# Performance work log

Measured on AMD Instinct MI355X. Metric: run time of the kernel, lower is better.

## Reference

```python
import jax, jax.numpy as jnp
import numpy as np

T, H, S = 131072, 768, 16384
MAX_LEN = 32


def setup_inputs() -> dict:
    key = jax.random.key(0)
    k1, k2, k3, k4 = jax.random.split(key, 4)
    token_emb = jax.random.normal(k1, (T, H), dtype=jnp.float32)
    # spans: start in [0, T-MAX_LEN), length in [1, MAX_LEN], end exclusive
    starts = jax.random.randint(k2, (S,), 0, T - MAX_LEN)
    lengths = jax.random.randint(k3, (S,), 1, MAX_LEN + 1)
    spans = jnp.stack([starts, starts + lengths], axis=1).astype(jnp.int64)
    kw1, kw2 = jax.random.split(k4)
    W1 = jax.random.normal(kw1, (3 * H, H), dtype=jnp.float32) * (1.0 / np.sqrt(3 * H))
    b1 = jnp.zeros((H,), dtype=jnp.float32)
    W2 = jax.random.normal(kw2, (H, H), dtype=jnp.float32) * (1.0 / np.sqrt(H))
    b2 = jnp.zeros((H,), dtype=jnp.float32)
    return {"token_emb": token_emb, "spans": spans, "W1": W1, "b1": b1, "W2": W2, "b2": b2}


def reference(token_emb, spans, W1, b1, W2, b2):
    starts = spans[:, 0]          # [S]
    ends = spans[:, 1]           # [S], exclusive
    h_start = token_emb[starts]   # [S, H]
    h_end = token_emb[ends - 1]   # [S, H]
    # ragged mean over h[s:e] via exclusive-prefix-sum difference
    zeros = jnp.zeros((1, token_emb.shape[1]), dtype=token_emb.dtype)
    cs = jnp.concatenate([zeros, jnp.cumsum(token_emb, axis=0)], axis=0)  # [T+1, H]
    lengths = (ends - starts).astype(token_emb.dtype)[:, None]            # [S, 1]
    h_mean = (cs[ends] - cs[starts]) / lengths                            # [S, H]
    feat = jnp.concatenate([h_start, h_end, h_mean], axis=-1)            # [S, 3H]
    # span_proj: Linear(3H->H) + GELU (dropout = identity at eval)
    z = jax.nn.gelu(feat @ W1 + b1, approximate=False)
    # projector: Linear(H->proj_dim) + GELU
    return jax.nn.gelu(z @ W2 + b2, approximate=False)
```

## Files before the change

kernel.cpp:

```cpp
#include <hip/hip_runtime.h>
#include <hip/hip_bf16.h>
#include <math.h>

#define H_DIM   768
#define S_SPAN  16384
#define K1_DIM  2304

typedef __attribute__((ext_vector_type(8))) short short8;
typedef __attribute__((ext_vector_type(4))) float floatx4;

__device__ __forceinline__ float gelu_exact(float x) {
    return 0.5f * x * (1.0f + erff(x * 0.70710678118654752f));
}

__device__ __forceinline__ void async_ld16(const __hip_bfloat16* g, __hip_bfloat16* l) {
    __builtin_amdgcn_global_load_lds(
        (const __attribute__((address_space(1))) void*)g,
        (__attribute__((address_space(3))) void*)l, 16, 0, 0);
}

__device__ __forceinline__ void store_out(float* p, float v) { *p = v; }
__device__ __forceinline__ void store_out(__hip_bfloat16* p, float v) { *p = __float2bfloat16(v); }

__global__ void transpose_to_bf16(const float* __restrict__ src,
                                  __hip_bfloat16* __restrict__ dst,
                                  int K, int N) {
    __shared__ float tile[32][33];
    const int nb = blockIdx.x * 32;
    const int kb = blockIdx.y * 32;
    const int tx = threadIdx.x;
    const int ty = threadIdx.y;
#pragma unroll
    for (int i = ty; i < 32; i += 8)
        tile[i][tx] = src[(size_t)(kb + i) * N + nb + tx];
    __syncthreads();
#pragma unroll
    for (int i = ty; i < 32; i += 8)
        dst[(size_t)(nb + i) * K + kb + tx] = __float2bfloat16(tile[tx][i]);
}

__global__ __launch_bounds__(192)
void gather_feat(const float* __restrict__ emb,
                 const int* __restrict__ spans,
                 __hip_bfloat16* __restrict__ feat) {
    const int s = blockIdx.x;
    const int st = spans[2 * s];
    const int en = spans[2 * s + 1];
    const int len = en - st;
    const int t = threadIdx.x;

    const float4* p = (const float4*)(emb + (size_t)st * H_DIM) + t;
    float4 v = *p;
    float4 first = v;
    float4 last = v;
    float sx = v.x, sy = v.y, sz = v.z, sw = v.w;
    for (int i = 1; i < len; ++i) {
        p += (H_DIM / 4);
        v = *p;
        sx += v.x; sy += v.y; sz += v.z; sw += v.w;
        last = v;
    }
    const float inv = 1.0f / (float)len;

    __hip_bfloat16* f = feat + (size_t)s * K1_DIM + 4 * t;
    union { __hip_bfloat16 h[4]; uint2 u; } pk;
    pk.h[0] = __float2bfloat16(first.x); pk.h[1] = __float2bfloat16(first.y);
    pk.h[2] = __float2bfloat16(first.z); pk.h[3] = __float2bfloat16(first.w);
    *(uint2*)(f) = pk.u;
    pk.h[0] = __float2bfloat16(last.x);  pk.h[1] = __float2bfloat16(last.y);
    pk.h[2] = __float2bfloat16(last.z);  pk.h[3] = __float2bfloat16(last.w);
    *(uint2*)(f + H_DIM) = pk.u;
    pk.h[0] = __float2bfloat16(sx * inv); pk.h[1] = __float2bfloat16(sy * inv);
    pk.h[2] = __float2bfloat16(sz * inv); pk.h[3] = __float2bfloat16(sw * inv);
    *(uint2*)(f + 2 * H_DIM) = pk.u;
}

template <typename OutT>
__global__ __launch_bounds__(256, 3)
void gemm_bias_gelu(const __hip_bfloat16* __restrict__ A,
                    const __hip_bfloat16* __restrict__ Bt,
                    const float* __restrict__ bias,
                    OutT* __restrict__ C,
                    int M, int N, int K) {
    __shared__ __align__(16) __hip_bfloat16 sA[128 * 32];
    __shared__ __align__(16) __hip_bfloat16 sB[128 * 32];

    const int tid  = threadIdx.x;
    const int wave = tid >> 6;
    const int lane = tid & 63;
    const int waveM = (wave >> 1) * 64;
    const int waveN = (wave & 1) * 64;

    const int tm0 = blockIdx.y * 128;
    const int tn0 = blockIdx.x * 128;

    const __hip_bfloat16* Abase = A + (size_t)tm0 * K;
    const __hip_bfloat16* Bbase = Bt + (size_t)tn0 * K;

    const int srow = wave * 32 + (lane >> 2);
    const int skof = (lane & 3) * 8;
    const __hip_bfloat16* gA0 = Abase + (size_t)srow * K + skof;
    const __hip_bfloat16* gA1 = gA0 + (size_t)16 * K;
    const __hip_bfloat16* gB0 = Bbase + (size_t)srow * K + skof;
    const __hip_bfloat16* gB1 = gB0 + (size_t)16 * K;
    __hip_bfloat16* lA0 = &sA[wave * 1024];
    __hip_bfloat16* lA1 = &sA[wave * 1024 + 512];
    __hip_bfloat16* lB0 = &sB[wave * 1024];
    __hip_bfloat16* lB1 = &sB[wave * 1024 + 512];

    floatx4 acc[4][4] = {};

    const int fr = lane & 15;
    const int fq = (lane >> 4) * 8;

    for (int k0 = 0; k0 < K; k0 += 32) {
        __syncthreads();
        async_ld16(gA0 + k0, lA0);
        async_ld16(gA1 + k0, lA1);
        async_ld16(gB0 + k0, lB0);
        async_ld16(gB1 + k0, lB1);
        __syncthreads();

        short8 af[4], bfr[4];
#pragma unroll
        for (int i = 0; i < 4; ++i) {
            af[i]  = *(const short8*)&sA[(waveM + i * 16 + fr) * 32 + fq];
            bfr[i] = *(const short8*)&sB[(waveN + i * 16 + fr) * 32 + fq];
        }
#pragma unroll
        for (int mi = 0; mi < 4; ++mi)
#pragma unroll
            for (int ni = 0; ni < 4; ++ni)
                acc[mi][ni] = __builtin_amdgcn_mfma_f32_16x16x32_bf16(
                    af[mi], bfr[ni], acc[mi][ni], 0, 0, 0);
    }

    const int col = lane & 15;
    const int rq  = (lane >> 4) * 4;
#pragma unroll
    for (int ni = 0; ni < 4; ++ni) {
        const int gc = tn0 + waveN + ni * 16 + col;
        const float bv = bias[gc];
#pragma unroll
        for (int mi = 0; mi < 4; ++mi) {
#pragma unroll
            for (int r = 0; r < 4; ++r) {
                const int gr = tm0 + waveM + mi * 16 + rq + r;
                store_out(&C[(size_t)gr * N + gc], gelu_exact(acc[mi][ni][r] + bv));
            }
        }
    }
}

extern "C" void kernel_launch(void* const* d_in, const int* in_sizes, int n_in,
                              void* d_out, int out_size, void* d_ws, size_t ws_size,
                              hipStream_t stream) {
    const float* token_emb = (const float*)d_in[0];
    const int*   spans     = (const int*)d_in[1];
    const float* W1        = (const float*)d_in[2];
    const float* b1        = (const float*)d_in[3];
    const float* W2        = (const float*)d_in[4];
    const float* b2        = (const float*)d_in[5];
    float*       out       = (float*)d_out;

    __hip_bfloat16* W1t  = (__hip_bfloat16*)d_ws;
    __hip_bfloat16* W2t  = W1t  + (size_t)H_DIM * K1_DIM;
    __hip_bfloat16* feat = W2t  + (size_t)H_DIM * H_DIM;
    __hip_bfloat16* z    = feat + (size_t)S_SPAN * K1_DIM;

    transpose_to_bf16<<<dim3(H_DIM / 32, K1_DIM / 32), dim3(32, 8), 0, stream>>>(
        W1, W1t, K1_DIM, H_DIM);
    transpose_to_bf16<<<dim3(H_DIM / 32, H_DIM / 32), dim3(32, 8), 0, stream>>>(
        W2, W2t, H_DIM, H_DIM);
    gather_feat<<<S_SPAN, 192, 0, stream>>>(token_emb, spans, feat);
    gemm_bias_gelu<__hip_bfloat16><<<dim3(H_DIM / 128, S_SPAN / 128), 256, 0, stream>>>(
        feat, W1t, b1, z, S_SPAN, H_DIM, K1_DIM);
    gemm_bias_gelu<float><<<dim3(H_DIM / 128, S_SPAN / 128), 256, 0, stream>>>(
        z, W2t, b2, out, S_SPAN, H_DIM, H_DIM);
}
```

Measured before the change: 728.1 us.

## Use one wave per span in gather with prefetch, and remap GEMM blocks across XCDs

The gather kernel now gives each span a single 64-lane wave that handles three float4 per lane, and software-prefetches the next row while accumulating the current one. This gives each thread more independent loads in flight and cuts the number of blocks launched. The GEMM swizzles the linear block id so that consecutive blocks on the same XCD cover neighbouring M rows and share all N tiles, which is meant to improve L2 reuse of the A panels. The prefetch always reads one row past the span end; with the input generation used here that row stays inside the table, but it is an extra load.

```diff
diff --git a/kernel.cpp b/kernel.cpp
--- a/kernel.cpp
+++ b/kernel.cpp
@@ -39,40 +39,55 @@
         dst[(size_t)(nb + i) * K + kb + tx] = __float2bfloat16(tile[tx][i]);
 }
 
-__global__ __launch_bounds__(192)
+__device__ __forceinline__ void store_row3(__hip_bfloat16* f, int lane,
+                                           float4 v0, float4 v1, float4 v2) {
+    union { __hip_bfloat16 h[4]; uint2 u; } pk;
+    pk.h[0] = __float2bfloat16(v0.x); pk.h[1] = __float2bfloat16(v0.y);
+    pk.h[2] = __float2bfloat16(v0.z); pk.h[3] = __float2bfloat16(v0.w);
+    *(uint2*)(f + 4 * lane) = pk.u;
+    pk.h[0] = __float2bfloat16(v1.x); pk.h[1] = __float2bfloat16(v1.y);
+    pk.h[2] = __float2bfloat16(v1.z); pk.h[3] = __float2bfloat16(v1.w);
+    *(uint2*)(f + 4 * (lane + 64)) = pk.u;
+    pk.h[0] = __float2bfloat16(v2.x); pk.h[1] = __float2bfloat16(v2.y);
+    pk.h[2] = __float2bfloat16(v2.z); pk.h[3] = __float2bfloat16(v2.w);
+    *(uint2*)(f + 4 * (lane + 128)) = pk.u;
+}
+
+__global__ __launch_bounds__(256)
 void gather_feat(const float* __restrict__ emb,
                  const int* __restrict__ spans,
                  __hip_bfloat16* __restrict__ feat) {
-    const int s = blockIdx.x;
-    const int st = spans[2 * s];
-    const int en = spans[2 * s + 1];
-    const int len = en - st;
-    const int t = threadIdx.x;
+    const int s    = blockIdx.x * 4 + (threadIdx.x >> 6);
+    const int lane = threadIdx.x & 63;
+    const int st   = spans[2 * s];
+    const int len  = spans[2 * s + 1] - st;
 
-    const float4* p = (const float4*)(emb + (size_t)st * H_DIM) + t;
-    float4 v = *p;
-    float4 first = v;
-    float4 last = v;
-    float sx = v.x, sy = v.y, sz = v.z, sw = v.w;
+    const float4* r = (const float4*)(emb + (size_t)st * H_DIM);
+    float4 a0 = r[lane], a1 = r[lane + 64], a2 = r[lane + 128];
+
+    __hip_bfloat16* f = feat + (size_t)s * K1_DIM;
+    store_row3(f, lane, a0, a1, a2);
+
+    float4 s0 = a0, s1 = a1, s2 = a2;
+    r += H_DIM / 4;
+    float4 n0 = r[lane], n1 = r[lane + 64], n2 = r[lane + 128];
+
     for (int i = 1; i < len; ++i) {
-        p += (H_DIM / 4);
-        v = *p;
-        sx += v.x; sy += v.y; sz += v.z; sw += v.w;
-        last = v;
+        a0 = n0; a1 = n1; a2 = n2;
+        r += H_DIM / 4;
+        n0 = r[lane]; n1 = r[lane + 64]; n2 = r[lane + 128];
+        s0.x += a0.x; s0.y += a0.y; s0.z += a0.z; s0.w += a0.w;
+        s1.x += a1.x; s1.y += a1.y; s1.z += a1.z; s1.w += a1.w;
+        s2.x += a2.x; s2.y += a2.y; s2.z += a2.z; s2.w += a2.w;
     }
+
+    store_row3(f + H_DIM, lane, a0, a1, a2);
+
     const float inv = 1.0f / (float)len;
-
-    __hip_bfloat16* f = feat + (size_t)s * K1_DIM + 4 * t;
-    union { __hip_bfloat16 h[4]; uint2 u; } pk;
-    pk.h[0] = __float2bfloat16(first.x); pk.h[1] = __float2bfloat16(first.y);
-    pk.h[2] = __float2bfloat16(first.z); pk.h[3] = __float2bfloat16(first.w);
-    *(uint2*)(f) = pk.u;
-    pk.h[0] = __float2bfloat16(last.x);  pk.h[1] = __float2bfloat16(last.y);
-    pk.h[2] = __float2bfloat16(last.z);  pk.h[3] = __float2bfloat16(last.w);
-    *(uint2*)(f + H_DIM) = pk.u;
-    pk.h[0] = __float2bfloat16(sx * inv); pk.h[1] = __float2bfloat16(sy * inv);
-    pk.h[2] = __float2bfloat16(sz * inv); pk.h[3] = __float2bfloat16(sw * inv);
-    *(uint2*)(f + 2 * H_DIM) = pk.u;
+    s0.x *= inv; s0.y *= inv; s0.z *= inv; s0.w *= inv;
+    s1.x *= inv; s1.y *= inv; s1.z *= inv; s1.w *= inv;
+    s2.x *= inv; s2.y *= inv; s2.z *= inv; s2.w *= inv;
+    store_row3(f + 2 * H_DIM, lane, s0, s1, s2);
 }
 
 template <typename OutT>
@@ -91,8 +106,12 @@
     const int waveM = (wave >> 1) * 64;
     const int waveN = (wave & 1) * 64;
 
-    const int tm0 = blockIdx.y * 128;
-    const int tn0 = blockIdx.x * 128;
+    const unsigned nbx = gridDim.x;
+    unsigned lin = blockIdx.y * nbx + blockIdx.x;
+    const unsigned chunk = (nbx * gridDim.y) >> 3;
+    lin = (lin & 7) * chunk + (lin >> 3);
+    const int tm0 = (int)(lin / nbx) * 128;
+    const int tn0 = (int)(lin % nbx) * 128;
 
     const __hip_bfloat16* Abase = A + (size_t)tm0 * K;
     const __hip_bfloat16* Bbase = Bt + (size_t)tn0 * K;
@@ -172,7 +191,7 @@
         W1, W1t, K1_DIM, H_DIM);
     transpose_to_bf16<<<dim3(H_DIM / 32, H_DIM / 32), dim3(32, 8), 0, stream>>>(
         W2, W2t, H_DIM, H_DIM);
-    gather_feat<<<S_SPAN, 192, 0, stream>>>(token_emb, spans, feat);
+    gather_feat<<<S_SPAN / 4, 256, 0, stream>>>(token_emb, spans, feat);
     gemm_bias_gelu<__hip_bfloat16><<<dim3(H_DIM / 128, S_SPAN / 128), 256, 0, stream>>>(
         feat, W1t, b1, z, S_SPAN, H_DIM, K1_DIM);
     gemm_bias_gelu<float><<<dim3(H_DIM / 128, S_SPAN / 128), 256, 0, stream>>>(
```

Result: no change. 722.9 us (-0.7%).
